# Kernel optimization log

Hardware: AMD Instinct MI355X
Metric: run time of the kernel (lower is better)

## Reference

```python
import jax, jax.numpy as jnp
import numpy as np

N = 100000      # nodes
E = 1600000     # edges
F_IN = 128
HID = 64
N_CLS = 40


def setup_inputs() -> dict:
    key = jax.random.key(0)
    ks = jax.random.split(key, 8)
    x = jax.random.normal(ks[0], (N, F_IN), dtype=jnp.float32)
    edge_index = jax.random.randint(ks[1], (2, E), 0, N, dtype=jnp.int64)
    # SAGEConv params: lin_l (applied to mean-aggregated neighbors, with bias),
    # lin_r (applied to root/self features, no bias). Glorot-ish init scaling.
    W1_l = jax.random.normal(ks[2], (F_IN, HID), dtype=jnp.float32) / np.sqrt(F_IN)
    b1 = jnp.zeros((HID,), dtype=jnp.float32)
    W1_r = jax.random.normal(ks[3], (F_IN, HID), dtype=jnp.float32) / np.sqrt(F_IN)
    W2_l = jax.random.normal(ks[4], (HID, N_CLS), dtype=jnp.float32) / np.sqrt(HID)
    b2 = jnp.zeros((N_CLS,), dtype=jnp.float32)
    W2_r = jax.random.normal(ks[5], (HID, N_CLS), dtype=jnp.float32) / np.sqrt(HID)
    return {"x": x, "edge_index": edge_index,
            "W1_l": W1_l, "b1": b1, "W1_r": W1_r,
            "W2_l": W2_l, "b2": b2, "W2_r": W2_r}


def _sage_conv(x, src, dst, W_l, b_l, W_r):
    # mean aggregation of neighbor features: messages flow src -> dst
    msgs = x[src]                                              # [E, d]
    summed = jax.ops.segment_sum(msgs, dst, num_segments=N)    # [N, d]
    cnt = jax.ops.segment_sum(jnp.ones((src.shape[0],), x.dtype), dst,
                              num_segments=N)                  # [N]
    agg = summed / jnp.maximum(cnt, 1.0)[:, None]
    return agg @ W_l + b_l + x @ W_r


def reference(x, edge_index, W1_l, b1, W1_r, W2_l, b2, W2_r):
    src, dst = edge_index[0], edge_index[1]
    h = jax.nn.relu(_sage_conv(x, src, dst, W1_l, b1, W1_r))
    # dropout: identity in eval mode
    logits = _sage_conv(h, src, dst, W2_l, b2, W2_r)
    return jax.nn.log_softmax(logits, axis=1)
```

## Files before the change

kernel.cpp:

```cpp
#include <hip/hip_runtime.h>
#include <math.h>

#define N_NODES 100000
#define F_IN    128
#define HID     64
#define N_CLS   40
#define MT      (N_NODES / 16)

#define BSHIFT  9
#define BSZ     512
#define NB      ((N_NODES + BSZ - 1) / BSZ)
#define EPB     4096

typedef __attribute__((ext_vector_type(8))) short bf8_t;
typedef __attribute__((ext_vector_type(4))) float f4_t;
typedef __attribute__((ext_vector_type(2))) float f2v_t;

typedef unsigned short ushort_t;
typedef unsigned int uint_t;
typedef unsigned char uchar_t;

__device__ __forceinline__ ushort_t f2b(float f) {
    union { float f; uint_t u; } c; c.f = f;
    uint_t u = c.u + 0x7FFFu + ((c.u >> 16) & 1u);
    return (ushort_t)(u >> 16);
}
__device__ __forceinline__ float b2f(ushort_t h) {
    union { uint_t u; float f; } c; c.u = ((uint_t)h) << 16;
    return c.f;
}

#if defined(__has_builtin)
#if __has_builtin(__builtin_amdgcn_cvt_pk_f32_fp8) && __has_builtin(__builtin_amdgcn_cvt_pk_fp8_f32)
#define HAVE_FP8_HW 1
#endif
#endif

__device__ __forceinline__ uchar_t fp8_enc(float v) {
#ifdef HAVE_FP8_HW
    return (uchar_t)(__builtin_amdgcn_cvt_pk_fp8_f32(v, v, 0, false) & 0xff);
#else
    union { float f; uint_t u; } c; c.f = v;
    uint_t s = c.u >> 31;
    float av = fabsf(v);
    if (av > 448.f) av = 448.f;
    int e;
    float m = frexpf(av, &e);
    int ee = e + 6;
    uchar_t r;
    if (av == 0.f) r = 0;
    else if (ee <= 0) {
        int q = (int)(av * 512.f + 0.5f);
        if (q > 7) q = 7;
        r = (uchar_t)q;
    } else {
        int q = (int)(m * 16.f + 0.5f);
        if (q == 16) { q = 8; ee += 1; }
        if (ee > 15) { ee = 15; q = 15; }
        r = (uchar_t)((ee << 3) | (q & 7));
    }
    return r | (uchar_t)(s << 7);
#endif
}

__device__ __forceinline__ f2v_t fp8x2_dec_lo(uint_t w) {
#ifdef HAVE_FP8_HW
    return __builtin_amdgcn_cvt_pk_f32_fp8(w, false);
#else
    f2v_t r;
    for (int k = 0; k < 2; ++k) {
        uchar_t b = (w >> (8 * k)) & 0xff;
        uint_t s = (b >> 7) & 1, e = (b >> 3) & 15, m = b & 7;
        float f;
        if (e) { union { uint_t u; float ff; } c;
                 c.u = (s << 31) | ((e + 120) << 23) | (m << 20); f = c.ff; }
        else   { f = (float)m * 0.001953125f; if (s) f = -f; }
        r[k] = f;
    }
    return r;
#endif
}
__device__ __forceinline__ f2v_t fp8x2_dec_hi(uint_t w) {
#ifdef HAVE_FP8_HW
    return __builtin_amdgcn_cvt_pk_f32_fp8(w, true);
#else
    return fp8x2_dec_lo(w >> 16);
#endif
}

__global__ void block_hist_kernel(const int* __restrict__ ei, int E,
                                  int* __restrict__ blockHist) {
    __shared__ int cnt[NB];
    int t = threadIdx.x, blk = blockIdx.x;
    for (int i = t; i < NB; i += 256) cnt[i] = 0;
    __syncthreads();
    int e0 = blk * EPB;
#pragma unroll
    for (int i = 0; i < EPB / 256; ++i) {
        int e = e0 + i * 256 + t;
        if (e < E) atomicAdd(&cnt[ei[E + e] >> BSHIFT], 1);
    }
    __syncthreads();
    for (int i = t; i < NB; i += 256) blockHist[blk * NB + i] = cnt[i];
}

__global__ void col_scan_kernel(const int* __restrict__ blockHist, int nblk,
                                int* __restrict__ blockBase,
                                int* __restrict__ btot) {
    __shared__ int ss[256];
    __shared__ int carry;
    int bin = blockIdx.x, t = threadIdx.x;
    if (t == 0) carry = 0;
    __syncthreads();
    for (int c0 = 0; c0 < nblk; c0 += 256) {
        int b = c0 + t;
        int v = (b < nblk) ? blockHist[b * NB + bin] : 0;
        ss[t] = v;
        __syncthreads();
        for (int off = 1; off < 256; off <<= 1) {
            int u = (t >= off) ? ss[t - off] : 0;
            __syncthreads();
            ss[t] += u;
            __syncthreads();
        }
        if (b < nblk) blockBase[b * NB + bin] = carry + ss[t] - v;
        __syncthreads();
        if (t == 255) carry += ss[255];
        __syncthreads();
    }
    if (t == 0) btot[bin] = carry;
}

__global__ void scatter_pairs_kernel(const int* __restrict__ ei, int E,
                                     const int* __restrict__ blockBase,
                                     const int* __restrict__ btot,
                                     uint_t* __restrict__ pairs) {
    __shared__ int cur[NB];
    __shared__ int base[NB];
    __shared__ int ss[256];
    int t = threadIdx.x, blk = blockIdx.x;
    int v = (t < NB) ? btot[t] : 0;
    ss[t] = v;
    __syncthreads();
    for (int off = 1; off < 256; off <<= 1) {
        int u = (t >= off) ? ss[t - off] : 0;
        __syncthreads();
        ss[t] += u;
        __syncthreads();
    }
    if (t < NB) {
        cur[t] = 0;
        base[t] = (ss[t] - v) + blockBase[blk * NB + t];
    }
    __syncthreads();
    int e0 = blk * EPB;
#pragma unroll
    for (int i = 0; i < EPB / 256; ++i) {
        int e = e0 + i * 256 + t;
        if (e < E) {
            int src = ei[e];
            int dst = ei[E + e];
            int bin = dst >> BSHIFT;
            int r = atomicAdd(&cur[bin], 1);
            pairs[base[bin] + r] = ((uint_t)src << BSHIFT) | (uint_t)(dst & (BSZ - 1));
        }
    }
}

__global__ void bucket_sort_kernel(const uint_t* __restrict__ pairs,
                                   const int* __restrict__ btot,
                                   int* __restrict__ rowptr,
                                   int* __restrict__ csr) {
    __shared__ int hist[BSZ];
    __shared__ int lofs[BSZ];
    int bin = blockIdx.x, t = threadIdx.x;
    int pv = (t < NB) ? btot[t] : 0;
    lofs[t] = pv;
    __syncthreads();
    for (int off = 1; off < BSZ; off <<= 1) {
        int u = (t >= off) ? lofs[t - off] : 0;
        __syncthreads();
        lofs[t] += u;
        __syncthreads();
    }
    int base = (bin > 0) ? lofs[bin - 1] : 0;
    int cnt = btot[bin];
    __syncthreads();
    hist[t] = 0;
    __syncthreads();
    for (int i = t; i < cnt; i += BSZ)
        atomicAdd(&hist[pairs[base + i] & (BSZ - 1)], 1);
    __syncthreads();
    int v = hist[t];
    lofs[t] = v;
    __syncthreads();
    for (int off = 1; off < BSZ; off <<= 1) {
        int u = (t >= off) ? lofs[t - off] : 0;
        __syncthreads();
        lofs[t] += u;
        __syncthreads();
    }
    int excl = lofs[t] - v;
    int d_global = (bin << BSHIFT) + t;
    if (d_global < N_NODES) rowptr[d_global] = base + excl;
    if (bin == NB - 1 && t == 0) rowptr[N_NODES] = base + cnt;
    __syncthreads();
    lofs[t] = excl;
    hist[t] = 0;
    __syncthreads();
    for (int i = t; i < cnt; i += BSZ) {
        uint_t p = pairs[base + i];
        int lb = p & (BSZ - 1);
        int r = atomicAdd(&hist[lb], 1);
        csr[base + lofs[lb] + r] = (int)(p >> BSHIFT);
    }
}

__global__ void cvt_w_kernel(const float* __restrict__ W1l,
                             const float* __restrict__ W1r,
                             const float* __restrict__ W2l,
                             const float* __restrict__ W2r,
                             ushort_t* __restrict__ W1t,
                             ushort_t* __restrict__ W2t) {
    int t = blockIdx.x * blockDim.x + threadIdx.x;
    if (t < 128 * F_IN) {
        int n = t / F_IN, k = t - n * F_IN;
        float v = (n < HID) ? W1l[k * HID + n] : W1r[k * HID + (n - HID)];
        W1t[t] = f2b(v);
    } else if (t < 128 * F_IN + 80 * HID) {
        int u = t - 128 * F_IN;
        int n = u / HID, k = u - n * HID;
        float v = (n < N_CLS) ? W2l[k * N_CLS + n] : W2r[k * N_CLS + (n - N_CLS)];
        W2t[u] = f2b(v);
    }
}

__global__ void gemm1_mfma_kernel(const float* __restrict__ x,
                                  const ushort_t* __restrict__ W1t,
                                  uchar_t* __restrict__ y1f8,
                                  ushort_t* __restrict__ z1b) {
    __shared__ uchar_t sy[128][80];
    __shared__ ushort_t sz[128][72];
    int tid = threadIdx.x;
    int wave = tid >> 6, lane = tid & 63;
    int tile0 = blockIdx.x * 8 + wave * 2;
    int m0b = blockIdx.x * 128;
    int r = lane & 15, q = lane >> 4;
    bool v0 = (tile0 < MT), v1 = (tile0 + 1 < MT);

    bf8_t a0[4], a1[4];
#pragma unroll
    for (int kt = 0; kt < 4; ++kt) { a0[kt] = (bf8_t)(short)0; a1[kt] = (bf8_t)(short)0; }
    if (v0) {
        const float* xr = x + (size_t)(tile0 * 16 + r) * F_IN + q * 8;
#pragma unroll
        for (int kt = 0; kt < 4; ++kt) {
            float4 u = *(const float4*)(xr + kt * 32);
            float4 v = *(const float4*)(xr + kt * 32 + 4);
            bf8_t tt;
            tt[0] = (short)f2b(u.x); tt[1] = (short)f2b(u.y);
            tt[2] = (short)f2b(u.z); tt[3] = (short)f2b(u.w);
            tt[4] = (short)f2b(v.x); tt[5] = (short)f2b(v.y);
            tt[6] = (short)f2b(v.z); tt[7] = (short)f2b(v.w);
            a0[kt] = tt;
        }
    }
    if (v1) {
        const float* xr = x + (size_t)((tile0 + 1) * 16 + r) * F_IN + q * 8;
#pragma unroll
        for (int kt = 0; kt < 4; ++kt) {
            float4 u = *(const float4*)(xr + kt * 32);
            float4 v = *(const float4*)(xr + kt * 32 + 4);
            bf8_t tt;
            tt[0] = (short)f2b(u.x); tt[1] = (short)f2b(u.y);
            tt[2] = (short)f2b(u.z); tt[3] = (short)f2b(u.w);
            tt[4] = (short)f2b(v.x); tt[5] = (short)f2b(v.y);
            tt[6] = (short)f2b(v.z); tt[7] = (short)f2b(v.w);
            a1[kt] = tt;
        }
    }
    int lr0 = wave * 32 + q * 4;
#pragma unroll
    for (int tn = 0; tn < 8; ++tn) {
        const ushort_t* wr = W1t + (size_t)(tn * 16 + r) * F_IN + q * 8;
        bf8_t b[4];
#pragma unroll
        for (int kt = 0; kt < 4; ++kt)
            b[kt] = *(const bf8_t*)(wr + kt * 32);
        f4_t acc0 = {0.f, 0.f, 0.f, 0.f};
        f4_t acc1 = {0.f, 0.f, 0.f, 0.f};
#pragma unroll
        for (int kt = 0; kt < 4; ++kt) {
            acc0 = __builtin_amdgcn_mfma_f32_16x16x32_bf16(a0[kt], b[kt], acc0, 0, 0, 0);
            acc1 = __builtin_amdgcn_mfma_f32_16x16x32_bf16(a1[kt], b[kt], acc1, 0, 0, 0);
        }
        int col = tn * 16 + r;
        if (col < 64) {
            if (v0) {
#pragma unroll
                for (int rr = 0; rr < 4; ++rr) sy[lr0 + rr][col] = fp8_enc(acc0[rr]);
            }
            if (v1) {
#pragma unroll
                for (int rr = 0; rr < 4; ++rr) sy[lr0 + 16 + rr][col] = fp8_enc(acc1[rr]);
            }
        } else {
            if (v0) {
#pragma unroll
                for (int rr = 0; rr < 4; ++rr) sz[lr0 + rr][col - 64] = f2b(acc0[rr]);
            }
            if (v1) {
#pragma unroll
                for (int rr = 0; rr < 4; ++rr) sz[lr0 + 16 + rr][col - 64] = f2b(acc1[rr]);
            }
        }
    }
    __syncthreads();
    int vrows = N_NODES - m0b; if (vrows > 128) vrows = 128;
    for (int idx = tid; idx < vrows * 4; idx += 256) {
        int row = idx >> 2, c = (idx & 3) << 4;
        *(uint4*)(y1f8 + (size_t)(m0b + row) * 64 + c) = *(const uint4*)&sy[row][c];
    }
    for (int idx = tid; idx < vrows * 8; idx += 256) {
        int row = idx >> 3, c = (idx & 7) << 3;
        *(uint4*)(z1b + (size_t)(m0b + row) * HID + c) = *(const uint4*)&sz[row][c];
    }
}

__device__ __forceinline__ void acc16(float* acc, uint4 v) {
    f2v_t p;
    p = fp8x2_dec_lo(v.x); acc[0]  += p[0]; acc[1]  += p[1];
    p = fp8x2_dec_hi(v.x); acc[2]  += p[0]; acc[3]  += p[1];
    p = fp8x2_dec_lo(v.y); acc[4]  += p[0]; acc[5]  += p[1];
    p = fp8x2_dec_hi(v.y); acc[6]  += p[0]; acc[7]  += p[1];
    p = fp8x2_dec_lo(v.z); acc[8]  += p[0]; acc[9]  += p[1];
    p = fp8x2_dec_hi(v.z); acc[10] += p[0]; acc[11] += p[1];
    p = fp8x2_dec_lo(v.w); acc[12] += p[0]; acc[13] += p[1];
    p = fp8x2_dec_hi(v.w); acc[14] += p[0]; acc[15] += p[1];
}

__global__ void agg1_kernel(const int* __restrict__ rowptr,
                            const int* __restrict__ csr,
                            const uchar_t* __restrict__ y1f8,
                            const ushort_t* __restrict__ z1b,
                            const float* __restrict__ b1,
                            ushort_t* __restrict__ hb) {
    int gid = blockIdx.x * blockDim.x + threadIdx.x;
    int wave = gid >> 6, lane = gid & 63;
    int g = lane >> 2, l = lane & 3;
    int n = wave * 16 + g;
    if (n >= N_NODES) return;
    int beg = rowptr[n], end = rowptr[n + 1];
    float acc[16];
#pragma unroll
    for (int j = 0; j < 16; ++j) acc[j] = 0.f;
    const uchar_t* yb = y1f8 + l * 16;
    int i = beg;
    for (; i + 3 < end; i += 4) {
        int s0 = csr[i], s1 = csr[i + 1], s2 = csr[i + 2], s3 = csr[i + 3];
        uint4 w0 = *(const uint4*)(yb + (size_t)s0 * 64);
        uint4 w1 = *(const uint4*)(yb + (size_t)s1 * 64);
        uint4 w2 = *(const uint4*)(yb + (size_t)s2 * 64);
        uint4 w3 = *(const uint4*)(yb + (size_t)s3 * 64);
        acc16(acc, w0); acc16(acc, w1); acc16(acc, w2); acc16(acc, w3);
    }
    for (; i < end; ++i) {
        uint4 w = *(const uint4*)(yb + (size_t)csr[i] * 64);
        acc16(acc, w);
    }
    float inv = 1.0f / fmaxf((float)(end - beg), 1.0f);
    int c = l * 16;
    ushort_t zz[16];
    *(uint4*)&zz[0] = *(const uint4*)(z1b + (size_t)n * HID + c);
    *(uint4*)&zz[8] = *(const uint4*)(z1b + (size_t)n * HID + c + 8);
    float bv[16];
    *(float4*)&bv[0]  = *(const float4*)(b1 + c);
    *(float4*)&bv[4]  = *(const float4*)(b1 + c + 4);
    *(float4*)&bv[8]  = *(const float4*)(b1 + c + 8);
    *(float4*)&bv[12] = *(const float4*)(b1 + c + 12);
    ushort_t o[16];
#pragma unroll
    for (int j = 0; j < 16; ++j) {
        float r = fmaxf(fmaf(acc[j], inv, bv[j] + b2f(zz[j])), 0.f);
        o[j] = f2b(r);
    }
    *(uint4*)(hb + (size_t)n * HID + c)     = *(const uint4*)&o[0];
    *(uint4*)(hb + (size_t)n * HID + c + 8) = *(const uint4*)&o[8];
}

__global__ void gemm2_mfma_kernel(const ushort_t* __restrict__ hb,
                                  const ushort_t* __restrict__ W2t,
                                  uchar_t* __restrict__ y2f8,
                                  ushort_t* __restrict__ z2b) {
    __shared__ uchar_t sy2[64 * 40];
    __shared__ ushort_t sz2[64][56];
    int tid = threadIdx.x;
    int wave = tid >> 6, lane = tid & 63;
    int tile = blockIdx.x * 4 + wave;
    int m0b = blockIdx.x * 64;
    if (tile < MT) {
        int m0 = tile * 16;
        int r = lane & 15, q = lane >> 4;
        const ushort_t* hr = hb + (size_t)(m0 + r) * HID + q * 8;
        bf8_t a[2];
#pragma unroll
        for (int kt = 0; kt < 2; ++kt)
            a[kt] = *(const bf8_t*)(hr + kt * 32);
        int lr0 = wave * 16 + q * 4;
#pragma unroll
        for (int tn = 0; tn < 5; ++tn) {
            const ushort_t* wr = W2t + (size_t)(tn * 16 + r) * HID + q * 8;
            f4_t acc = {0.f, 0.f, 0.f, 0.f};
#pragma unroll
            for (int kt = 0; kt < 2; ++kt) {
                bf8_t b = *(const bf8_t*)(wr + kt * 32);
                acc = __builtin_amdgcn_mfma_f32_16x16x32_bf16(a[kt], b, acc, 0, 0, 0);
            }
            int col = tn * 16 + r;
            if (col < N_CLS) {
#pragma unroll
                for (int rr = 0; rr < 4; ++rr)
                    sy2[(lr0 + rr) * 40 + col] = fp8_enc(acc[rr]);
            } else {
#pragma unroll
                for (int rr = 0; rr < 4; ++rr)
                    sz2[lr0 + rr][col - N_CLS] = f2b(acc[rr]);
            }
        }
    }
    __syncthreads();
    int vrows = N_NODES - m0b; if (vrows > 64) vrows = 64;
    int nch = (vrows * 40) >> 4;
    for (int idx = tid; idx < nch; idx += 256)
        *(uint4*)(y2f8 + (size_t)m0b * 40 + idx * 16) = *(const uint4*)&sy2[idx * 16];
    for (int idx = tid; idx < vrows * 5; idx += 256) {
        int row = idx / 5, c = (idx - row * 5) * 8;
        *(uint4*)(z2b + (size_t)(m0b + row) * HID + c) = *(const uint4*)&sz2[row][c];
    }
}

__global__ void agg2_kernel(const int* __restrict__ rowptr,
                            const int* __restrict__ csr,
                            const uchar_t* __restrict__ y2f8,
                            const ushort_t* __restrict__ z2b,
                            const float* __restrict__ b2,
                            float* __restrict__ out) {
    int gid = blockIdx.x * blockDim.x + threadIdx.x;
    int wave = gid >> 6, lane = gid & 63;
    int g = lane >> 4, l = lane & 15;
    int n = wave * 4 + g;
    if (n >= N_NODES) return;
    int beg = rowptr[n], end = rowptr[n + 1];
    float a0 = 0.f, a1 = 0.f, a2 = 0.f, a3 = 0.f;
    float4 bb = make_float4(0.f, 0.f, 0.f, 0.f);
    ushort4 zz; zz.x = 0; zz.y = 0; zz.z = 0; zz.w = 0;
    int c0 = l * 4;
    if (l < 10) {
        int i = beg;
        for (; i + 7 < end; i += 8) {
            int s0 = csr[i],     s1 = csr[i + 1], s2 = csr[i + 2], s3 = csr[i + 3];
            int s4 = csr[i + 4], s5 = csr[i + 5], s6 = csr[i + 6], s7 = csr[i + 7];
            uint_t w0 = *(const uint_t*)(y2f8 + (size_t)s0 * 40 + c0);
            uint_t w1 = *(const uint_t*)(y2f8 + (size_t)s1 * 40 + c0);
            uint_t w2 = *(const uint_t*)(y2f8 + (size_t)s2 * 40 + c0);
            uint_t w3 = *(const uint_t*)(y2f8 + (size_t)s3 * 40 + c0);
            uint_t w4 = *(const uint_t*)(y2f8 + (size_t)s4 * 40 + c0);
            uint_t w5 = *(const uint_t*)(y2f8 + (size_t)s5 * 40 + c0);
            uint_t w6 = *(const uint_t*)(y2f8 + (size_t)s6 * 40 + c0);
            uint_t w7 = *(const uint_t*)(y2f8 + (size_t)s7 * 40 + c0);
            f2v_t p;
            p = fp8x2_dec_lo(w0); a0 += p[0]; a1 += p[1];
            p = fp8x2_dec_hi(w0); a2 += p[0]; a3 += p[1];
            p = fp8x2_dec_lo(w1); a0 += p[0]; a1 += p[1];
            p = fp8x2_dec_hi(w1); a2 += p[0]; a3 += p[1];
            p = fp8x2_dec_lo(w2); a0 += p[0]; a1 += p[1];
            p = fp8x2_dec_hi(w2); a2 += p[0]; a3 += p[1];
            p = fp8x2_dec_lo(w3); a0 += p[0]; a1 += p[1];
            p = fp8x2_dec_hi(w3); a2 += p[0]; a3 += p[1];
            p = fp8x2_dec_lo(w4); a0 += p[0]; a1 += p[1];
            p = fp8x2_dec_hi(w4); a2 += p[0]; a3 += p[1];
            p = fp8x2_dec_lo(w5); a0 += p[0]; a1 += p[1];
            p = fp8x2_dec_hi(w5); a2 += p[0]; a3 += p[1];
            p = fp8x2_dec_lo(w6); a0 += p[0]; a1 += p[1];
            p = fp8x2_dec_hi(w6); a2 += p[0]; a3 += p[1];
            p = fp8x2_dec_lo(w7); a0 += p[0]; a1 += p[1];
            p = fp8x2_dec_hi(w7); a2 += p[0]; a3 += p[1];
        }
        for (; i + 3 < end; i += 4) {
            int s0 = csr[i], s1 = csr[i + 1], s2 = csr[i + 2], s3 = csr[i + 3];
            uint_t w0 = *(const uint_t*)(y2f8 + (size_t)s0 * 40 + c0);
            uint_t w1 = *(const uint_t*)(y2f8 + (size_t)s1 * 40 + c0);
            uint_t w2 = *(const uint_t*)(y2f8 + (size_t)s2 * 40 + c0);
            uint_t w3 = *(const uint_t*)(y2f8 + (size_t)s3 * 40 + c0);
            f2v_t p;
            p = fp8x2_dec_lo(w0); a0 += p[0]; a1 += p[1];
            p = fp8x2_dec_hi(w0); a2 += p[0]; a3 += p[1];
            p = fp8x2_dec_lo(w1); a0 += p[0]; a1 += p[1];
            p = fp8x2_dec_hi(w1); a2 += p[0]; a3 += p[1];
            p = fp8x2_dec_lo(w2); a0 += p[0]; a1 += p[1];
            p = fp8x2_dec_hi(w2); a2 += p[0]; a3 += p[1];
            p = fp8x2_dec_lo(w3); a0 += p[0]; a1 += p[1];
            p = fp8x2_dec_hi(w3); a2 += p[0]; a3 += p[1];
        }
        for (; i < end; ++i) {
            uint_t w = *(const uint_t*)(y2f8 + (size_t)csr[i] * 40 + c0);
            f2v_t p0 = fp8x2_dec_lo(w), p1 = fp8x2_dec_hi(w);
            a0 += p0[0]; a1 += p0[1]; a2 += p1[0]; a3 += p1[1];
        }
        bb = *(const float4*)(b2 + c0);
        zz = *(const ushort4*)(z2b + (size_t)n * HID + c0);
    }
    float inv = 1.0f / fmaxf((float)(end - beg), 1.0f);
    float v0 = (c0 + 0 < N_CLS) ? fmaf(a0, inv, bb.x + b2f(zz.x)) : -INFINITY;
    float v1 = (c0 + 1 < N_CLS) ? fmaf(a1, inv, bb.y + b2f(zz.y)) : -INFINITY;
    float v2 = (c0 + 2 < N_CLS) ? fmaf(a2, inv, bb.z + b2f(zz.z)) : -INFINITY;
    float v3 = (c0 + 3 < N_CLS) ? fmaf(a3, inv, bb.w + b2f(zz.w)) : -INFINITY;

    float m = fmaxf(fmaxf(v0, v1), fmaxf(v2, v3));
#pragma unroll
    for (int off = 1; off < 16; off <<= 1)
        m = fmaxf(m, __shfl_xor(m, off, 64));
    float s = 0.f;
    if (v0 > -INFINITY) s += expf(v0 - m);
    if (v1 > -INFINITY) s += expf(v1 - m);
    if (v2 > -INFINITY) s += expf(v2 - m);
    if (v3 > -INFINITY) s += expf(v3 - m);
#pragma unroll
    for (int off = 1; off < 16; off <<= 1)
        s += __shfl_xor(s, off, 64);
    float ls = logf(s);
    if (l < 10) {
        float4 o = make_float4(v0 - m - ls, v1 - m - ls, v2 - m - ls, v3 - m - ls);
        *(float4*)(out + (size_t)n * N_CLS + c0) = o;
    }
}

extern "C" void kernel_launch(void* const* d_in, const int* in_sizes, int n_in,
                              void* d_out, int out_size, void* d_ws, size_t ws_size,
                              hipStream_t stream) {
    const float* x   = (const float*)d_in[0];
    const int*   ei  = (const int*)d_in[1];
    const float* W1l = (const float*)d_in[2];
    const float* b1  = (const float*)d_in[3];
    const float* W1r = (const float*)d_in[4];
    const float* W2l = (const float*)d_in[5];
    const float* b2  = (const float*)d_in[6];
    const float* W2r = (const float*)d_in[7];
    float* out = (float*)d_out;
    const int E = in_sizes[1] / 2;
    const int nblk = (E + EPB - 1) / EPB;

    char* p = (char*)d_ws;
    auto take = [&](size_t bytes) {
        char* q = p;
        p += (bytes + 15) & ~(size_t)15;
        return (void*)q;
    };
    int* rowptr     = (int*)take(sizeof(int) * (N_NODES + 4));
    int* blockHist  = (int*)take(sizeof(int) * (size_t)nblk * NB);
    int* blockBase  = (int*)take(sizeof(int) * (size_t)nblk * NB);
    int* btot       = (int*)take(sizeof(int) * NB);
    uint_t* pairs   = (uint_t*)take(sizeof(uint_t) * (size_t)E);
    int* csr        = (int*)take(sizeof(int) * (size_t)E);
    ushort_t* W1t   = (ushort_t*)take(sizeof(ushort_t) * 128 * F_IN);
    ushort_t* W2t   = (ushort_t*)take(sizeof(ushort_t) * 80 * HID);
    uchar_t* y1f8   = (uchar_t*)take(sizeof(uchar_t) * (size_t)N_NODES * 64);
    ushort_t* z1b   = (ushort_t*)take(sizeof(ushort_t) * (size_t)N_NODES * HID);
    ushort_t* hb    = (ushort_t*)take(sizeof(ushort_t) * (size_t)N_NODES * HID);
    uchar_t* y2f8 = y1f8;
    ushort_t* z2b = z1b;

    const int B = 256;

    block_hist_kernel<<<nblk, 256, 0, stream>>>(ei, E, blockHist);
    col_scan_kernel<<<NB, 256, 0, stream>>>(blockHist, nblk, blockBase, btot);
    scatter_pairs_kernel<<<nblk, 256, 0, stream>>>(ei, E, blockBase, btot, pairs);
    bucket_sort_kernel<<<NB, BSZ, 0, stream>>>(pairs, btot, rowptr, csr);

    cvt_w_kernel<<<(128 * F_IN + 80 * HID + B - 1) / B, B, 0, stream>>>(
        W1l, W1r, W2l, W2r, W1t, W2t);

    int gemm1_blocks = (MT + 7) / 8;
    int gemm2_blocks = (MT + 3) / 4;
    int t_agg1 = (N_NODES / 16) * 64;
    int t_agg2 = (N_NODES / 4) * 64;

    gemm1_mfma_kernel<<<gemm1_blocks, B, 0, stream>>>(x, W1t, y1f8, z1b);
    agg1_kernel<<<(t_agg1 + B - 1) / B, B, 0, stream>>>(rowptr, csr, y1f8, z1b, b1, hb);
    gemm2_mfma_kernel<<<gemm2_blocks, B, 0, stream>>>(hb, W2t, y2f8, z2b);
    agg2_kernel<<<(t_agg2 + B - 1) / B, B, 0, stream>>>(rowptr, csr, y2f8, z2b, b2, out);
}
```

Baseline: 232.8 us.

## Aggregate hidden features before layer-2 GEMM and fuse log_softmax into GEMM

```diff
diff --git a/kernel.cpp b/kernel.cpp
--- a/kernel.cpp
+++ b/kernel.cpp
@@ -344,7 +344,8 @@
                             const uchar_t* __restrict__ y1f8,
                             const ushort_t* __restrict__ z1b,
                             const float* __restrict__ b1,
-                            ushort_t* __restrict__ hb) {
+                            ushort_t* __restrict__ hb,
+                            uchar_t* __restrict__ hf8) {
     int gid = blockIdx.x * blockDim.x + threadIdx.x;
     int wave = gid >> 6, lane = gid & 63;
     int g = lane >> 2, l = lane & 3;
@@ -379,21 +380,61 @@
     *(float4*)&bv[8]  = *(const float4*)(b1 + c + 8);
     *(float4*)&bv[12] = *(const float4*)(b1 + c + 12);
     ushort_t o[16];
+    uchar_t of[16];
 #pragma unroll
     for (int j = 0; j < 16; ++j) {
         float r = fmaxf(fmaf(acc[j], inv, bv[j] + b2f(zz[j])), 0.f);
         o[j] = f2b(r);
+        of[j] = fp8_enc(r);
     }
     *(uint4*)(hb + (size_t)n * HID + c)     = *(const uint4*)&o[0];
     *(uint4*)(hb + (size_t)n * HID + c + 8) = *(const uint4*)&o[8];
-}
-
-__global__ void gemm2_mfma_kernel(const ushort_t* __restrict__ hb,
-                                  const ushort_t* __restrict__ W2t,
-                                  uchar_t* __restrict__ y2f8,
-                                  ushort_t* __restrict__ z2b) {
-    __shared__ uchar_t sy2[64 * 40];
-    __shared__ ushort_t sz2[64][56];
+    *(uint4*)(hf8 + (size_t)n * 64 + c)     = *(const uint4*)&of[0];
+}
+
+__global__ void agg2m_kernel(const int* __restrict__ rowptr,
+                             const int* __restrict__ csr,
+                             const uchar_t* __restrict__ hf8,
+                             ushort_t* __restrict__ mb) {
+    int gid = blockIdx.x * blockDim.x + threadIdx.x;
+    int wave = gid >> 6, lane = gid & 63;
+    int g = lane >> 2, l = lane & 3;
+    int n = wave * 16 + g;
+    if (n >= N_NODES) return;
+    int beg = rowptr[n], end = rowptr[n + 1];
+    float acc[16];
+#pragma unroll
+    for (int j = 0; j < 16; ++j) acc[j] = 0.f;
+    const uchar_t* yb = hf8 + l * 16;
+    int i = beg;
+    for (; i + 3 < end; i += 4) {
+        int s0 = csr[i], s1 = csr[i + 1], s2 = csr[i + 2], s3 = csr[i + 3];
+        uint4 w0 = *(const uint4*)(yb + (size_t)s0 * 64);
+        uint4 w1 = *(const uint4*)(yb + (size_t)s1 * 64);
+        uint4 w2 = *(const uint4*)(yb + (size_t)s2 * 64);
+        uint4 w3 = *(const uint4*)(yb + (size_t)s3 * 64);
+        acc16(acc, w0); acc16(acc, w1); acc16(acc, w2); acc16(acc, w3);
+    }
+    for (; i < end; ++i) {
+        uint4 w = *(const uint4*)(yb + (size_t)csr[i] * 64);
+        acc16(acc, w);
+    }
+    float inv = 1.0f / fmaxf((float)(end - beg), 1.0f);
+    int c = l * 16;
+    ushort_t o[16];
+#pragma unroll
+    for (int j = 0; j < 16; ++j)
+        o[j] = f2b(acc[j] * inv);
+    *(uint4*)(mb + (size_t)n * HID + c)     = *(const uint4*)&o[0];
+    *(uint4*)(mb + (size_t)n * HID + c + 8) = *(const uint4*)&o[8];
+}
+
+__global__ void gemm2_fused_kernel(const ushort_t* __restrict__ mb,
+                                   const ushort_t* __restrict__ hb,
+                                   const ushort_t* __restrict__ W2t,
+                                   const float* __restrict__ b2,
+                                   float* __restrict__ out) {
+    __shared__ float sOut[64][44];
     int tid = threadIdx.x;
     int wave = tid >> 6, lane = tid & 63;
     int tile = blockIdx.x * 4 + wave;
@@ -401,137 +442,65 @@
     if (tile < MT) {
         int m0 = tile * 16;
         int r = lane & 15, q = lane >> 4;
+        const ushort_t* mr = mb + (size_t)(m0 + r) * HID + q * 8;
         const ushort_t* hr = hb + (size_t)(m0 + r) * HID + q * 8;
-        bf8_t a[2];
-#pragma unroll
-        for (int kt = 0; kt < 2; ++kt)
-            a[kt] = *(const bf8_t*)(hr + kt * 32);
-        int lr0 = wave * 16 + q * 4;
-#pragma unroll
-        for (int tn = 0; tn < 5; ++tn) {
-            const ushort_t* wr = W2t + (size_t)(tn * 16 + r) * HID + q * 8;
+        bf8_t a0[2], a1[2];
+#pragma unroll
+        for (int kt = 0; kt < 2; ++kt) {
+            a0[kt] = *(const bf8_t*)(mr + kt * 32);
+            a1[kt] = *(const bf8_t*)(hr + kt * 32);
+        }
+        float v[3][4];
+#pragma unroll
+        for (int tn = 0; tn < 3; ++tn) {
+            int col = tn * 16 + r;
+            int cl = (col < N_CLS) ? col : 0;
+            const ushort_t* wl = W2t + (size_t)cl * HID + q * 8;
+            const ushort_t* wrp = W2t + (size_t)(N_CLS + cl) * HID + q * 8;
             f4_t acc = {0.f, 0.f, 0.f, 0.f};
 #pragma unroll
             for (int kt = 0; kt < 2; ++kt) {
-                bf8_t b = *(const bf8_t*)(wr + kt * 32);
-                acc = __builtin_amdgcn_mfma_f32_16x16x32_bf16(a[kt], b, acc, 0, 0, 0);
-            }
-            int col = tn * 16 + r;
-            if (col < N_CLS) {
-#pragma unroll
-                for (int rr = 0; rr < 4; ++rr)
-                    sy2[(lr0 + rr) * 40 + col] = fp8_enc(acc[rr]);
-            } else {
-#pragma unroll
-                for (int rr = 0; rr < 4; ++rr)
-                    sz2[lr0 + rr][col - N_CLS] = f2b(acc[rr]);
+                bf8_t bl = *(const bf8_t*)(wl + kt * 32);
+                acc = __builtin_amdgcn_mfma_f32_16x16x32_bf16(a0[kt], bl, acc, 0, 0, 0);
+            }
+#pragma unroll
+            for (int kt = 0; kt < 2; ++kt) {
+                bf8_t br = *(const bf8_t*)(wrp + kt * 32);
+                acc = __builtin_amdgcn_mfma_f32_16x16x32_bf16(a1[kt], br, acc, 0, 0, 0);
+            }
+            float bias = (col < N_CLS) ? b2[cl] : 0.f;
+#pragma unroll
+            for (int rr = 0; rr < 4; ++rr)
+                v[tn][rr] = (col < N_CLS) ? (acc[rr] + bias) : -INFINITY;
+        }
+        int lrow = wave * 16 + q * 4;
+#pragma unroll
+        for (int rr = 0; rr < 4; ++rr) {
+            float m = fmaxf(fmaxf(v[0][rr], v[1][rr]), v[2][rr]);
+#pragma unroll
+            for (int off = 1; off < 16; off <<= 1)
+                m = fmaxf(m, __shfl_xor(m, off, 64));
+            float s = 0.f;
+#pragma unroll
+            for (int tn = 0; tn < 3; ++tn)
+                if (v[tn][rr] > -INFINITY) s += expf(v[tn][rr] - m);
+#pragma unroll
+            for (int off = 1; off < 16; off <<= 1)
+                s += __shfl_xor(s, off, 64);
+            float ls = m + logf(s);
+#pragma unroll
+            for (int tn = 0; tn < 3; ++tn) {
+                int col = tn * 16 + r;
+                if (col < N_CLS)
+                    sOut[lrow + rr][col] = v[tn][rr] - ls;
             }
         }
     }
     __syncthreads();
     int vrows = N_NODES - m0b; if (vrows > 64) vrows = 64;
-    int nch = (vrows * 40) >> 4;
-    for (int idx = tid; idx < nch; idx += 256)
-        *(uint4*)(y2f8 + (size_t)m0b * 40 + idx * 16) = *(const uint4*)&sy2[idx * 16];
-    for (int idx = tid; idx < vrows * 5; idx += 256) {
-        int row = idx / 5, c = (idx - row * 5) * 8;
-        *(uint4*)(z2b + (size_t)(m0b + row) * HID + c) = *(const uint4*)&sz2[row][c];
-    }
-}
-
-__global__ void agg2_kernel(const int* __restrict__ rowptr,
-                            const int* __restrict__ csr,
-                            const uchar_t* __restrict__ y2f8,
-                            const ushort_t* __restrict__ z2b,
-                            const float* __restrict__ b2,
-                            float* __restrict__ out) {
-    int gid = blockIdx.x * blockDim.x + threadIdx.x;
-    int wave = gid >> 6, lane = gid & 63;
-    int g = lane >> 4, l = lane & 15;
-    int n = wave * 4 + g;
-    if (n >= N_NODES) return;
-    int beg = rowptr[n], end = rowptr[n + 1];
-    float a0 = 0.f, a1 = 0.f, a2 = 0.f, a3 = 0.f;
-    float4 bb = make_float4(0.f, 0.f, 0.f, 0.f);
-    ushort4 zz; zz.x = 0; zz.y = 0; zz.z = 0; zz.w = 0;
-    int c0 = l * 4;
-    if (l < 10) {
-        int i = beg;
-        for (; i + 7 < end; i += 8) {
-            int s0 = csr[i],     s1 = csr[i + 1], s2 = csr[i + 2], s3 = csr[i + 3];
-            int s4 = csr[i + 4], s5 = csr[i + 5], s6 = csr[i + 6], s7 = csr[i + 7];
-            uint_t w0 = *(const uint_t*)(y2f8 + (size_t)s0 * 40 + c0);
-            uint_t w1 = *(const uint_t*)(y2f8 + (size_t)s1 * 40 + c0);
-            uint_t w2 = *(const uint_t*)(y2f8 + (size_t)s2 * 40 + c0);
-            uint_t w3 = *(const uint_t*)(y2f8 + (size_t)s3 * 40 + c0);
-            uint_t w4 = *(const uint_t*)(y2f8 + (size_t)s4 * 40 + c0);
-            uint_t w5 = *(const uint_t*)(y2f8 + (size_t)s5 * 40 + c0);
-            uint_t w6 = *(const uint_t*)(y2f8 + (size_t)s6 * 40 + c0);
-            uint_t w7 = *(const uint_t*)(y2f8 + (size_t)s7 * 40 + c0);
-            f2v_t p;
-            p = fp8x2_dec_lo(w0); a0 += p[0]; a1 += p[1];
-            p = fp8x2_dec_hi(w0); a2 += p[0]; a3 += p[1];
-            p = fp8x2_dec_lo(w1); a0 += p[0]; a1 += p[1];
-            p = fp8x2_dec_hi(w1); a2 += p[0]; a3 += p[1];
-            p = fp8x2_dec_lo(w2); a0 += p[0]; a1 += p[1];
-            p = fp8x2_dec_hi(w2); a2 += p[0]; a3 += p[1];
-            p = fp8x2_dec_lo(w3); a0 += p[0]; a1 += p[1];
-            p = fp8x2_dec_hi(w3); a2 += p[0]; a3 += p[1];
-            p = fp8x2_dec_lo(w4); a0 += p[0]; a1 += p[1];
-            p = fp8x2_dec_hi(w4); a2 += p[0]; a3 += p[1];
-            p = fp8x2_dec_lo(w5); a0 += p[0]; a1 += p[1];
-            p = fp8x2_dec_hi(w5); a2 += p[0]; a3 += p[1];
-            p = fp8x2_dec_lo(w6); a0 += p[0]; a1 += p[1];
-            p = fp8x2_dec_hi(w6); a2 += p[0]; a3 += p[1];
-            p = fp8x2_dec_lo(w7); a0 += p[0]; a1 += p[1];
-            p = fp8x2_dec_hi(w7); a2 += p[0]; a3 += p[1];
-        }
-        for (; i + 3 < end; i += 4) {
-            int s0 = csr[i], s1 = csr[i + 1], s2 = csr[i + 2], s3 = csr[i + 3];
-            uint_t w0 = *(const uint_t*)(y2f8 + (size_t)s0 * 40 + c0);
-            uint_t w1 = *(const uint_t*)(y2f8 + (size_t)s1 * 40 + c0);
-            uint_t w2 = *(const uint_t*)(y2f8 + (size_t)s2 * 40 + c0);
-            uint_t w3 = *(const uint_t*)(y2f8 + (size_t)s3 * 40 + c0);
-            f2v_t p;
-            p = fp8x2_dec_lo(w0); a0 += p[0]; a1 += p[1];
-            p = fp8x2_dec_hi(w0); a2 += p[0]; a3 += p[1];
-            p = fp8x2_dec_lo(w1); a0 += p[0]; a1 += p[1];
-            p = fp8x2_dec_hi(w1); a2 += p[0]; a3 += p[1];
-            p = fp8x2_dec_lo(w2); a0 += p[0]; a1 += p[1];
-            p = fp8x2_dec_hi(w2); a2 += p[0]; a3 += p[1];
-            p = fp8x2_dec_lo(w3); a0 += p[0]; a1 += p[1];
-            p = fp8x2_dec_hi(w3); a2 += p[0]; a3 += p[1];
-        }
-        for (; i < end; ++i) {
-            uint_t w = *(const uint_t*)(y2f8 + (size_t)csr[i] * 40 + c0);
-            f2v_t p0 = fp8x2_dec_lo(w), p1 = fp8x2_dec_hi(w);
-            a0 += p0[0]; a1 += p0[1]; a2 += p1[0]; a3 += p1[1];
-        }
-        bb = *(const float4*)(b2 + c0);
-        zz = *(const ushort4*)(z2b + (size_t)n * HID + c0);
-    }
-    float inv = 1.0f / fmaxf((float)(end - beg), 1.0f);
-    float v0 = (c0 + 0 < N_CLS) ? fmaf(a0, inv, bb.x + b2f(zz.x)) : -INFINITY;
-    float v1 = (c0 + 1 < N_CLS) ? fmaf(a1, inv, bb.y + b2f(zz.y)) : -INFINITY;
-    float v2 = (c0 + 2 < N_CLS) ? fmaf(a2, inv, bb.z + b2f(zz.z)) : -INFINITY;
-    float v3 = (c0 + 3 < N_CLS) ? fmaf(a3, inv, bb.w + b2f(zz.w)) : -INFINITY;
-
-    float m = fmaxf(fmaxf(v0, v1), fmaxf(v2, v3));
-#pragma unroll
-    for (int off = 1; off < 16; off <<= 1)
-        m = fmaxf(m, __shfl_xor(m, off, 64));
-    float s = 0.f;
-    if (v0 > -INFINITY) s += expf(v0 - m);
-    if (v1 > -INFINITY) s += expf(v1 - m);
-    if (v2 > -INFINITY) s += expf(v2 - m);
-    if (v3 > -INFINITY) s += expf(v3 - m);
-#pragma unroll
-    for (int off = 1; off < 16; off <<= 1)
-        s += __shfl_xor(s, off, 64);
-    float ls = logf(s);
-    if (l < 10) {
-        float4 o = make_float4(v0 - m - ls, v1 - m - ls, v2 - m - ls, v3 - m - ls);
-        *(float4*)(out + (size_t)n * N_CLS + c0) = o;
+    for (int idx = tid; idx < vrows * 10; idx += 256) {
+        int row = idx / 10, c = (idx - row * 10) * 4;
+        *(float4*)(out + (size_t)(m0b + row) * N_CLS + c) = *(const float4*)&sOut[row][c];
     }
 }
 
@@ -567,8 +536,8 @@
     uchar_t* y1f8   = (uchar_t*)take(sizeof(uchar_t) * (size_t)N_NODES * 64);
     ushort_t* z1b   = (ushort_t*)take(sizeof(ushort_t) * (size_t)N_NODES * HID);
     ushort_t* hb    = (ushort_t*)take(sizeof(ushort_t) * (size_t)N_NODES * HID);
-    uchar_t* y2f8 = y1f8;
-    ushort_t* z2b = z1b;
+    uchar_t* hf8    = (uchar_t*)take(sizeof(uchar_t) * (size_t)N_NODES * 64);
+    ushort_t* mb    = (ushort_t*)take(sizeof(ushort_t) * (size_t)N_NODES * HID);
 
     const int B = 256;
 
@@ -582,11 +551,10 @@
 
     int gemm1_blocks = (MT + 7) / 8;
     int gemm2_blocks = (MT + 3) / 4;
-    int t_agg1 = (N_NODES / 16) * 64;
-    int t_agg2 = (N_NODES / 4) * 64;
+    int t_agg = (N_NODES / 16) * 64;
 
     gemm1_mfma_kernel<<<gemm1_blocks, B, 0, stream>>>(x, W1t, y1f8, z1b);
-    agg1_kernel<<<(t_agg1 + B - 1) / B, B, 0, stream>>>(rowptr, csr, y1f8, z1b, b1, hb);
-    gemm2_mfma_kernel<<<gemm2_blocks, B, 0, stream>>>(hb, W2t, y2f8, z2b);
-    agg2_kernel<<<(t_agg2 + B - 1) / B, B, 0, stream>>>(rowptr, csr, y2f8, z2b, b2, out);
-}
+    agg1_kernel<<<(t_agg + B - 1) / B, B, 0, stream>>>(rowptr, csr, y1f8, z1b, b1, hb, hf8);
+    agg2m_kernel<<<(t_agg + B - 1) / B, B, 0, stream>>>(rowptr, csr, hf8, mb);
+    gemm2_fused_kernel<<<gemm2_blocks, B, 0, stream>>>(mb, hb, W2t, b2, out);
+}
```

Measured after the change: 232.1 us. About the same (-0.3%).
